# Performance work log

Measured on AMD Instinct MI355X. Metric: run time of the kernel, lower is better.

The kernel has to match this reference:

```python
import jax, jax.numpy as jnp
import numpy as np

B, CQ, CKV, E = 8, 256, 256, 256
H, W = 64, 64
HP, WP = 32, 32


def setup_inputs() -> dict:
    key = jax.random.key(0)
    ks = jax.random.split(key, 6)
    C = jax.random.normal(ks[0], (B, CQ, H, W), dtype=jnp.float32)
    P = jax.random.normal(ks[1], (B, CKV, HP, WP), dtype=jnp.float32)
    # 1x1 conv weights, kaiming-ish scale; stored as [out_ch, in_ch]
    theta_w = jax.random.normal(ks[2], (E, CQ), dtype=jnp.float32) * (1.0 / np.sqrt(CQ))
    phi_w = jax.random.normal(ks[3], (E, CKV), dtype=jnp.float32) * (1.0 / np.sqrt(CKV))
    g_w = jax.random.normal(ks[4], (E, CKV), dtype=jnp.float32) * (1.0 / np.sqrt(CKV))
    out_w = jax.random.normal(ks[5], (CQ, E), dtype=jnp.float32) * (1.0 / np.sqrt(E))
    return {"C": C, "P": P, "theta_w": theta_w, "phi_w": phi_w, "g_w": g_w, "out_w": out_w}


def reference(C, P, theta_w, phi_w, g_w, out_w):
    b, _, h, w = C.shape
    e = theta_w.shape[0]
    # 1x1 convs are channel GEMMs
    theta_C = jnp.einsum('bchw,ec->behw', C, theta_w).reshape(b, e, h * w)   # [B,E,Nq]
    phi_P = jnp.einsum('bchw,ec->behw', P, phi_w).reshape(b, e, -1)          # [B,E,Nkv]
    g_P = jnp.einsum('bchw,ec->behw', P, g_w).reshape(b, e, -1)              # [B,E,Nkv]
    attn = jnp.einsum('ben,bem->bnm', theta_C, phi_P) / (e ** 0.5)           # [B,Nq,Nkv]
    attn = jax.nn.softmax(attn, axis=-1)
    out = jnp.einsum('bem,bnm->ben', g_P, attn).reshape(b, e, h, w)          # [B,E,H,W]
    out = jnp.einsum('behw,ce->bchw', out, out_w)                            # [B,CQ,H,W]
    return jnp.concatenate([C, out], axis=1)
```

## Files before the change

kernel.cpp:

```cpp
#include <hip/hip_runtime.h>


typedef __attribute__((ext_vector_type(8))) short short8;
typedef __attribute__((ext_vector_type(16))) float f32x16;
typedef unsigned short ushort_t;

__device__ __forceinline__ unsigned short f2bf(float f) {
    unsigned int u = __float_as_uint(f);
    u += 0x7FFFu + ((u >> 16) & 1u);
    return (unsigned short)(u >> 16);
}
__device__ __forceinline__ unsigned int pack2bf(float a, float b) {
    return (unsigned int)f2bf(a) | ((unsigned int)f2bf(b) << 16);
}
__device__ __forceinline__ void gload16(const ushort_t* g, ushort_t* l) {
    __builtin_amdgcn_global_load_lds(
        (const __attribute__((address_space(1))) unsigned int*)g,
        (__attribute__((address_space(3))) unsigned int*)l, 16, 0, 0);
}
__device__ __forceinline__ f32x16 zero16() {
    f32x16 z;
#pragma unroll
    for (int i = 0; i < 16; ++i) z[i] = 0.f;
    return z;
}

__global__ __launch_bounds__(256) void ct_cvt(const float* __restrict__ X,
                                              float* __restrict__ outCopy,
                                              ushort_t* __restrict__ xT) {
    const int N = 4096;
    int b = blockIdx.z, c0 = blockIdx.y * 64, n0 = blockIdx.x * 64;
    int t = threadIdx.x;
    __shared__ float Xs[64][68];
    const float* Xb = X + ((size_t)b * 256 + c0) * N + n0;
    int cl = t >> 4, nl = (t & 15) * 4;
#pragma unroll
    for (int ci = 0; ci < 4; ++ci) {
        int c = ci * 16 + cl;
        float4 v = *(const float4*)(Xb + (size_t)c * N + nl);
        *(float4*)&Xs[c][nl] = v;
        *(float4*)(outCopy + (size_t)b * 2097152 + (size_t)(c0 + c) * N + n0 + nl) = v;
    }
    __syncthreads();
    ushort_t* xb = xT + (size_t)b * ((size_t)N * 256);
    int nl2 = t & 63, cgb = t >> 6;
#pragma unroll
    for (int cp = 0; cp < 2; ++cp) {
        int cg = cp * 4 + cgb;
        int cb = c0 + cg * 8;
        int n = n0 + nl2;
        short8 v;
#pragma unroll
        for (int u = 0; u < 8; ++u) v[u] = (short)f2bf(Xs[cg * 8 + u][nl2]);
        size_t i16 = ((size_t)(n >> 5) * 16 + (cb >> 4)) * 64 + ((cb >> 3) & 1) * 32 + (n & 31);
        *(short8*)(xb + i16 * 8) = v;
    }
}

__global__ __launch_bounds__(256) void prep_small(const float* __restrict__ P,
                                                  const float* __restrict__ thw,
                                                  const float* __restrict__ phw,
                                                  const float* __restrict__ ow,
                                                  const float* __restrict__ gw,
                                                  ushort_t* __restrict__ pT,
                                                  ushort_t* __restrict__ thc,
                                                  ushort_t* __restrict__ phc,
                                                  ushort_t* __restrict__ w2c) {
    int blk = blockIdx.x;
    int t = threadIdx.x;
    __shared__ float Xs[64][68];
    if (blk < 512) {
        const int N = 1024;
        int bx = blk & 15, by = (blk >> 4) & 3, b = blk >> 6;
        int n0 = bx * 64, c0 = by * 64;
        const float* Xb = P + ((size_t)b * 256 + c0) * N + n0;
        int cl = t >> 4, nl = (t & 15) * 4;
#pragma unroll
        for (int ci = 0; ci < 4; ++ci) {
            int c = ci * 16 + cl;
            *(float4*)&Xs[c][nl] = *(const float4*)(Xb + (size_t)c * N + nl);
        }
        __syncthreads();
        ushort_t* xb = pT + (size_t)b * ((size_t)N * 256);
        int nl2 = t & 63, cgb = t >> 6;
#pragma unroll
        for (int cp = 0; cp < 2; ++cp) {
            int cg = cp * 4 + cgb;
            int cb = c0 + cg * 8;
            int n = n0 + nl2;
            short8 v;
#pragma unroll
            for (int u = 0; u < 8; ++u) v[u] = (short)f2bf(Xs[cg * 8 + u][nl2]);
            size_t i16 = ((size_t)(n >> 5) * 16 + (cb >> 4)) * 64 + ((cb >> 3) & 1) * 32 + (n & 31);
            *(short8*)(xb + i16 * 8) = v;
        }
    } else if (blk < 1024) {
        int r = blk - 512;
        int which = r >> 8;
        int e = r & 255, c = t;
        const float* src = which ? phw : thw;
        ushort_t* dst = which ? phc : thc;
        int idx = ((((e >> 5) * 16 + (c >> 4)) * 64 + ((c >> 3) & 1) * 32 + (e & 31)) << 3) + (c & 7);
        dst[idx] = f2bf(src[e * 256 + c]);
    } else {
        int c0 = (blk - 1024) * 8;
        float acc[8] = {};
        for (int e = 0; e < 256; ++e) {
            float g = gw[e * 256 + t];
#pragma unroll
            for (int i = 0; i < 8; ++i) acc[i] += ow[(c0 + i) * 256 + e] * g;
        }
#pragma unroll
        for (int i = 0; i < 8; ++i) {
            int c = c0 + i, k = t;
            int idx = ((((c >> 5) * 16 + (k >> 4)) * 64 + ((k >> 3) & 1) * 32 + (c & 31)) << 3) + (k & 7);
            w2c[idx] = f2bf(acc[i]);
        }
    }
}

__global__ __launch_bounds__(256, 2) void proj_mfma(const ushort_t* __restrict__ thc,
                                                    const ushort_t* __restrict__ phc,
                                                    const ushort_t* __restrict__ w2c,
                                                    const ushort_t* __restrict__ cT,
                                                    const ushort_t* __restrict__ pT,
                                                    ushort_t* __restrict__ thetaA,
                                                    ushort_t* __restrict__ phiA,
                                                    ushort_t* __restrict__ gVx) {
    int blk = blockIdx.x;
    int tid = threadIdx.x, lane = tid & 63, wid = tid >> 6;
    int l31 = lane & 31, lh = lane >> 5;
    int role, b, nt;
    const ushort_t *Wc, *xTb;
    ushort_t* outp;
    float scale = 1.f;
    if (blk < 256) {
        role = 0; b = blk & 7; nt = blk >> 3;
        Wc = thc; xTb = cT + (size_t)b * 1048576; outp = thetaA + (size_t)b * 1048576;
        scale = 1.4426950408889634f / 16.0f;
    } else if (blk < 320) {
        int r = blk - 256; role = 1; b = r & 7; nt = r >> 3;
        Wc = phc; xTb = pT + (size_t)b * 262144; outp = phiA + (size_t)b * 262144;
    } else {
        int r = blk - 320; role = 2; b = r & 7; nt = r >> 3;
        Wc = w2c; xTb = pT + (size_t)b * 262144; outp = gVx + (size_t)b * 262144;
    }
    const int n0 = nt * 128 + wid * 32;
    const int ncr = (n0 >> 5) * 16;

    f32x16 o[8];
#pragma unroll
    for (int f = 0; f < 8; ++f) o[f] = zero16();

#pragma unroll
    for (int ks = 0; ks < 16; ++ks) {
        short8 xf = *(const short8*)(xTb + ((size_t)(ncr + ks) * 64 + lane) * 8);
#pragma unroll
        for (int f = 0; f < 8; ++f) {
            short8 wf = *(const short8*)(Wc + ((size_t)(f * 16 + ks) * 64 + lane) * 8);
            o[f] = __builtin_amdgcn_mfma_f32_32x32x16_bf16(wf, xf, o[f], 0, 0, 0);
        }
    }

    if (role < 2) {
#pragma unroll
        for (int f = 0; f < 8; ++f) {
#pragma unroll
            for (int rq = 0; rq < 4; ++rq) {
                uint2 st;
                st.x = pack2bf(o[f][4 * rq + 0] * scale, o[f][4 * rq + 1] * scale);
                st.y = pack2bf(o[f][4 * rq + 2] * scale, o[f][4 * rq + 3] * scale);
                size_t addr = ((size_t)(ncr + f * 2 + (rq >> 1)) * 64 + l31 + 32 * (rq & 1)) * 8 + 4 * lh;
                *(uint2*)(outp + addr) = st;
            }
        }
    } else {
        int kvq = (n0 >> 4) + (l31 >> 4);
        int lhw = 32 * ((l31 >> 3) & 1);
        int kl = l31 & 7;
#pragma unroll
        for (int f = 0; f < 8; ++f) {
#pragma unroll
            for (int r = 0; r < 16; ++r) {
                int crow = (r & 3) + 8 * (r >> 2) + 4 * lh;
                size_t addr = ((size_t)(f * 64 + kvq) * 64 + crow + lhw) * 8 + kl;
                outp[addr] = f2bf(o[f][r]);
            }
        }
    }
}

__global__ __launch_bounds__(512, 2) void attn4(const ushort_t* __restrict__ thetaA,
                                                const ushort_t* __restrict__ phiA,
                                                const ushort_t* __restrict__ gVx,
                                                float* __restrict__ out) {
    const int b = blockIdx.x & 7, qt = blockIdx.x >> 3;
    const int tid = threadIdx.x, lane = tid & 63, wid = tid >> 6;
    const int l31 = lane & 31, lh = lane >> 5;
    const int h = wid >> 2, qg = wid & 3;

    __shared__ __align__(16) ushort_t smem[65536];
    __shared__ float rmS[4][32], rlS[4][32];

    const ushort_t* thA = thetaA + (size_t)b * 1048576;
    const ushort_t* phA = phiA + (size_t)b * 262144;
    const ushort_t* gVb = gVx + (size_t)b * 262144;

    auto stage = [&](int it, int d) {
        if (wid < 2) {
            const ushort_t* src = phA + (size_t)(2 * it) * 8192 + (wid & 1) * 4096 + lane * 8;
            ushort_t* dst = smem + d * 8192 + (wid & 1) * 4096;
#pragma unroll
            for (int i = 0; i < 8; ++i) gload16(src + i * 512, dst + i * 512);
        } else if (wid < 4) {
#pragma unroll
            for (int cg2 = 0; cg2 < 4; ++cg2) {
                int cg = (wid & 1) * 4 + cg2;
#pragma unroll
                for (int j = 0; j < 2; ++j) {
                    const ushort_t* src = gVb + ((size_t)(cg * 64 + 4 * it + j) * 64 + lane) * 8;
                    ushort_t* dst = smem + 16384 + d * 8192 + cg * 1024 + j * 512;
                    gload16(src, dst);
                }
            }
        } else if (wid < 6) {
            const ushort_t* src = phA + (size_t)(2 * it + 1) * 8192 + (wid & 1) * 4096 + lane * 8;
            ushort_t* dst = smem + 32768 + d * 8192 + (wid & 1) * 4096;
#pragma unroll
            for (int i = 0; i < 8; ++i) gload16(src + i * 512, dst + i * 512);
        } else {
#pragma unroll
            for (int cg2 = 0; cg2 < 4; ++cg2) {
                int cg = (wid & 1) * 4 + cg2;
#pragma unroll
                for (int j = 0; j < 2; ++j) {
                    const ushort_t* src = gVb + ((size_t)(cg * 64 + 4 * it + 2 + j) * 64 + lane) * 8;
                    ushort_t* dst = smem + 32768 + 16384 + d * 8192 + cg * 1024 + j * 512;
                    gload16(src, dst);
                }
            }
        }
    };

    stage(0, 0);

    short8 qf[16];
    {
        const int qcr = (qt * 4 + qg) * 16;
#pragma unroll
        for (int ks = 0; ks < 16; ++ks)
            qf[ks] = *(const short8*)(thA + ((size_t)(qcr + ks) * 64 + lane) * 8);
    }

    f32x16 o[8];
#pragma unroll
    for (int f = 0; f < 8; ++f) o[f] = zero16();
    float rm = -1e30f, rl = 0.f;

    for (int it = 0; it < 16; ++it) {
        if (it < 15) {
            stage(it + 1, (it + 1) & 1);
            asm volatile("s_waitcnt vmcnt(8)" ::: "memory");
        } else {
            asm volatile("s_waitcnt vmcnt(0)" ::: "memory");
        }
        __builtin_amdgcn_s_barrier();
        __builtin_amdgcn_sched_barrier(0);

        const int d = it & 1;
        const ushort_t* Kb = smem + h * 32768 + d * 8192;
        const ushort_t* Vb = smem + h * 32768 + 16384 + d * 8192;

        f32x16 s = zero16();
#pragma unroll
        for (int ks = 0; ks < 16; ++ks) {
            short8 kf = *(const short8*)(Kb + (size_t)ks * 512 + lane * 8);
            s = __builtin_amdgcn_mfma_f32_32x32x16_bf16(kf, qf[ks], s, 0, 0, 0);
        }

        float tmax = s[0];
#pragma unroll
        for (int r = 1; r < 16; ++r) tmax = fmaxf(tmax, s[r]);
        tmax = fmaxf(tmax, __shfl_xor(tmax, 32));
        if (!__all(tmax - rm <= 8.f)) {
            float nm = fmaxf(rm, tmax);
            float sc = __builtin_amdgcn_exp2f(rm - nm);
            rl *= sc;
#pragma unroll
            for (int f = 0; f < 8; ++f)
#pragma unroll
                for (int r = 0; r < 16; ++r) o[f][r] *= sc;
            rm = nm;
        }
        float ps = 0.f;
#pragma unroll
        for (int r = 0; r < 16; ++r) {
            s[r] = __builtin_amdgcn_exp2f(s[r] - rm);
            ps += s[r];
        }
        ps += __shfl_xor(ps, 32);
        rl += ps;

        unsigned int a0 = pack2bf(s[0], s[1]),  b0 = pack2bf(s[4], s[5]);
        unsigned int a1 = pack2bf(s[2], s[3]),  b1 = pack2bf(s[6], s[7]);
        unsigned int a2 = pack2bf(s[8], s[9]),  b2 = pack2bf(s[12], s[13]);
        unsigned int a3 = pack2bf(s[10], s[11]), b3 = pack2bf(s[14], s[15]);
        asm volatile("v_permlane32_swap_b32 %0, %1" : "+v"(a0), "+v"(b0));
        asm volatile("v_permlane32_swap_b32 %0, %1" : "+v"(a1), "+v"(b1));
        asm volatile("v_permlane32_swap_b32 %0, %1" : "+v"(a2), "+v"(b2));
        asm volatile("v_permlane32_swap_b32 %0, %1" : "+v"(a3), "+v"(b3));
        union PW { unsigned int u[4]; short8 v; };
        PW p0; p0.u[0] = a0; p0.u[1] = a1; p0.u[2] = b0; p0.u[3] = b1;
        PW p1; p1.u[0] = a2; p1.u[1] = a3; p1.u[2] = b2; p1.u[3] = b3;

#pragma unroll
        for (int ks2 = 0; ks2 < 2; ++ks2) {
            short8 pf = ks2 ? p1.v : p0.v;
#pragma unroll
            for (int f = 0; f < 8; ++f) {
                short8 vf = *(const short8*)(Vb + (size_t)f * 1024 + ks2 * 512 + lane * 8);
                o[f] = __builtin_amdgcn_mfma_f32_32x32x16_bf16(vf, pf, o[f], 0, 0, 0);
            }
        }
        __builtin_amdgcn_sched_barrier(0);
        __builtin_amdgcn_s_barrier();
    }

    if (wid >= 4) {
        float* part = (float*)smem + (size_t)(wid - 4) * 8192;
#pragma unroll
        for (int f = 0; f < 8; ++f)
#pragma unroll
            for (int r = 0; r < 16; ++r) {
                int e = f * 32 + (r & 3) + 8 * (r >> 2) + 4 * lh;
                part[e * 32 + l31] = o[f][r];
            }
        if (lane < 32) { rmS[wid - 4][l31] = rm; rlS[wid - 4][l31] = rl; }
    }
    __syncthreads();
    if (wid < 4) {
        float rm1 = rmS[wid][l31], rl1 = rlS[wid][l31];
        float m = fmaxf(rm, rm1);
        float c0 = __builtin_amdgcn_exp2f(rm - m);
        float c1 = __builtin_amdgcn_exp2f(rm1 - m);
        float inv = 1.f / (rl * c0 + rl1 * c1);
        const float* part = (const float*)smem + (size_t)wid * 8192;
        float* ob = out + (size_t)b * 2097152 + (size_t)256 * 4096 + qt * 128 + qg * 32 + l31;
#pragma unroll
        for (int f = 0; f < 8; ++f)
#pragma unroll
            for (int r = 0; r < 16; ++r) {
                int e = f * 32 + (r & 3) + 8 * (r >> 2) + 4 * lh;
                ob[(size_t)e * 4096] = (o[f][r] * c0 + part[e * 32 + l31] * c1) * inv;
            }
    }
}


extern "C" void kernel_launch(void* const* d_in, const int* in_sizes, int n_in,
                              void* d_out, int out_size, void* d_ws, size_t ws_size,
                              hipStream_t stream) {
    const float* C       = (const float*)d_in[0];
    const float* P       = (const float*)d_in[1];
    const float* theta_w = (const float*)d_in[2];
    const float* phi_w   = (const float*)d_in[3];
    const float* g_w     = (const float*)d_in[4];
    const float* out_w   = (const float*)d_in[5];
    float* out = (float*)d_out;

    ushort_t* ws = (ushort_t*)d_ws;
    ushort_t* thetaA = ws;
    ushort_t* cT     = ws + 8388608;
    ushort_t* phiA   = ws + 16777216;
    ushort_t* pT     = ws + 18874368;
    ushort_t* gVx    = ws + 20971520;
    ushort_t* thWc   = ws + 23068672;
    ushort_t* phWc   = ws + 23134208;
    ushort_t* w2c    = ws + 23199744;

    prep_small<<<1056, 256, 0, stream>>>(P, theta_w, phi_w, out_w, g_w,
                                         pT, thWc, phWc, w2c);
    ct_cvt<<<dim3(64, 4, 8), 256, 0, stream>>>(C, out, cT);
    proj_mfma<<<384, 256, 0, stream>>>(thWc, phWc, w2c, cT, pT, thetaA, phiA, gVx);
    attn4<<<256, 512, 0, stream>>>(thetaA, phiA, gVx, out);
}
```

Before: 127.4 us.

## Software-pipeline QK of next tile with PV of current tile in attention

Restructures the attention kernel so the QK^T MFMAs for the next KV tile are computed one iteration ahead and interleaved with the PV MFMAs for the current tile. K and V staging become separate, with K prefetched two tiles ahead and V one tile ahead. The softmax work can then overlap the matrix units, and s_setprio raises wave priority during the MFMA section. In exchange it keeps an extra score accumulator live, which raises register pressure, and it uses one barrier per iteration with a full vmcnt(0) wait.

```diff
diff --git a/kernel.cpp b/kernel.cpp
--- a/kernel.cpp
+++ b/kernel.cpp
@@ -190,7 +190,7 @@
     }
 }
 
-__global__ __launch_bounds__(512, 2) void attn4(const ushort_t* __restrict__ thetaA,
+__global__ __launch_bounds__(512, 2) void attn6(const ushort_t* __restrict__ thetaA,
                                                 const ushort_t* __restrict__ phiA,
                                                 const ushort_t* __restrict__ gVx,
                                                 float* __restrict__ out) {
@@ -206,43 +206,33 @@
     const ushort_t* phA = phiA + (size_t)b * 262144;
     const ushort_t* gVb = gVx + (size_t)b * 262144;
 
-    auto stage = [&](int it, int d) {
-        if (wid < 2) {
-            const ushort_t* src = phA + (size_t)(2 * it) * 8192 + (wid & 1) * 4096 + lane * 8;
-            ushort_t* dst = smem + d * 8192 + (wid & 1) * 4096;
+    auto stageK = [&](int j) {
+        if ((wid & 2) == 0) {
+            int hh = wid >> 2;
+            const ushort_t* src = phA + (size_t)(2 * j + hh) * 8192 + (wid & 1) * 4096 + lane * 8;
+            ushort_t* dst = smem + hh * 16384 + (j & 1) * 8192 + (wid & 1) * 4096;
 #pragma unroll
             for (int i = 0; i < 8; ++i) gload16(src + i * 512, dst + i * 512);
-        } else if (wid < 4) {
+        }
+    };
+    auto stageV = [&](int j) {
+        if ((wid & 2) == 2) {
+            int hh = wid >> 2;
 #pragma unroll
             for (int cg2 = 0; cg2 < 4; ++cg2) {
                 int cg = (wid & 1) * 4 + cg2;
 #pragma unroll
-                for (int j = 0; j < 2; ++j) {
-                    const ushort_t* src = gVb + ((size_t)(cg * 64 + 4 * it + j) * 64 + lane) * 8;
-                    ushort_t* dst = smem + 16384 + d * 8192 + cg * 1024 + j * 512;
+                for (int jj = 0; jj < 2; ++jj) {
+                    const ushort_t* src =
+                        gVb + ((size_t)(cg * 64 + 4 * j + 2 * hh + jj) * 64 + lane) * 8;
+                    ushort_t* dst = smem + 32768 + hh * 16384 + (j & 1) * 8192 + cg * 1024 + jj * 512;
                     gload16(src, dst);
                 }
             }
-        } else if (wid < 6) {
-            const ushort_t* src = phA + (size_t)(2 * it + 1) * 8192 + (wid & 1) * 4096 + lane * 8;
-            ushort_t* dst = smem + 32768 + d * 8192 + (wid & 1) * 4096;
-#pragma unroll
-            for (int i = 0; i < 8; ++i) gload16(src + i * 512, dst + i * 512);
-        } else {
-#pragma unroll
-            for (int cg2 = 0; cg2 < 4; ++cg2) {
-                int cg = (wid & 1) * 4 + cg2;
-#pragma unroll
-                for (int j = 0; j < 2; ++j) {
-                    const ushort_t* src = gVb + ((size_t)(cg * 64 + 4 * it + 2 + j) * 64 + lane) * 8;
-                    ushort_t* dst = smem + 32768 + 16384 + d * 8192 + cg * 1024 + j * 512;
-                    gload16(src, dst);
-                }
-            }
         }
     };
 
-    stage(0, 0);
+    stageK(0); stageK(1); stageV(0);
 
     short8 qf[16];
     {
@@ -257,26 +247,26 @@
     for (int f = 0; f < 8; ++f) o[f] = zero16();
     float rm = -1e30f, rl = 0.f;
 
-    for (int it = 0; it < 16; ++it) {
-        if (it < 15) {
-            stage(it + 1, (it + 1) & 1);
-            asm volatile("s_waitcnt vmcnt(8)" ::: "memory");
-        } else {
-            asm volatile("s_waitcnt vmcnt(0)" ::: "memory");
-        }
-        __builtin_amdgcn_s_barrier();
-        __builtin_amdgcn_sched_barrier(0);
-
-        const int d = it & 1;
-        const ushort_t* Kb = smem + h * 32768 + d * 8192;
-        const ushort_t* Vb = smem + h * 32768 + 16384 + d * 8192;
-
-        f32x16 s = zero16();
+    asm volatile("s_waitcnt vmcnt(0)" ::: "memory");
+    __builtin_amdgcn_s_barrier();
+    __builtin_amdgcn_sched_barrier(0);
+
+    f32x16 s = zero16();
+    {
+        const ushort_t* Kb = smem + h * 16384;
 #pragma unroll
         for (int ks = 0; ks < 16; ++ks) {
             short8 kf = *(const short8*)(Kb + (size_t)ks * 512 + lane * 8);
             s = __builtin_amdgcn_mfma_f32_32x32x16_bf16(kf, qf[ks], s, 0, 0, 0);
         }
+    }
+
+    for (int it = 0; it < 16; ++it) {
+        asm volatile("s_waitcnt vmcnt(0)" ::: "memory");
+        __builtin_amdgcn_s_barrier();
+        __builtin_amdgcn_sched_barrier(0);
+        if (it < 14) stageK(it + 2);
+        if (it < 15) stageV(it + 1);
 
         float tmax = s[0];
 #pragma unroll
@@ -301,9 +291,9 @@
         ps += __shfl_xor(ps, 32);
         rl += ps;
 
-        unsigned int a0 = pack2bf(s[0], s[1]),  b0 = pack2bf(s[4], s[5]);
-        unsigned int a1 = pack2bf(s[2], s[3]),  b1 = pack2bf(s[6], s[7]);
-        unsigned int a2 = pack2bf(s[8], s[9]),  b2 = pack2bf(s[12], s[13]);
+        unsigned int a0 = pack2bf(s[0], s[1]),   b0 = pack2bf(s[4], s[5]);
+        unsigned int a1 = pack2bf(s[2], s[3]),   b1 = pack2bf(s[6], s[7]);
+        unsigned int a2 = pack2bf(s[8], s[9]),   b2 = pack2bf(s[12], s[13]);
         unsigned int a3 = pack2bf(s[10], s[11]), b3 = pack2bf(s[14], s[15]);
         asm volatile("v_permlane32_swap_b32 %0, %1" : "+v"(a0), "+v"(b0));
         asm volatile("v_permlane32_swap_b32 %0, %1" : "+v"(a1), "+v"(b1));
@@ -313,18 +303,40 @@
         PW p0; p0.u[0] = a0; p0.u[1] = a1; p0.u[2] = b0; p0.u[3] = b1;
         PW p1; p1.u[0] = a2; p1.u[1] = a3; p1.u[2] = b2; p1.u[3] = b3;
 
-#pragma unroll
-        for (int ks2 = 0; ks2 < 2; ++ks2) {
-            short8 pf = ks2 ? p1.v : p0.v;
-#pragma unroll
-            for (int f = 0; f < 8; ++f) {
-                short8 vf = *(const short8*)(Vb + (size_t)f * 1024 + ks2 * 512 + lane * 8);
-                o[f] = __builtin_amdgcn_mfma_f32_32x32x16_bf16(vf, pf, o[f], 0, 0, 0);
-            }
-        }
+        const ushort_t* Vb = smem + 32768 + h * 16384 + (it & 1) * 8192;
+        const ushort_t* Kb = smem + h * 16384 + ((it + 1) & 1) * 8192;
+        __builtin_amdgcn_s_setprio(1);
+        if (it < 15) {
+            f32x16 sn = zero16();
+#pragma unroll
+            for (int ks2 = 0; ks2 < 2; ++ks2) {
+                short8 pf = ks2 ? p1.v : p0.v;
+#pragma unroll
+                for (int f = 0; f < 8; ++f) {
+                    short8 vf = *(const short8*)(Vb + (size_t)f * 1024 + ks2 * 512 + lane * 8);
+                    o[f] = __builtin_amdgcn_mfma_f32_32x32x16_bf16(vf, pf, o[f], 0, 0, 0);
+                    int ks = ks2 * 8 + f;
+                    short8 kf = *(const short8*)(Kb + (size_t)ks * 512 + lane * 8);
+                    sn = __builtin_amdgcn_mfma_f32_32x32x16_bf16(kf, qf[ks], sn, 0, 0, 0);
+                }
+            }
+            s = sn;
+        } else {
+#pragma unroll
+            for (int ks2 = 0; ks2 < 2; ++ks2) {
+                short8 pf = ks2 ? p1.v : p0.v;
+#pragma unroll
+                for (int f = 0; f < 8; ++f) {
+                    short8 vf = *(const short8*)(Vb + (size_t)f * 1024 + ks2 * 512 + lane * 8);
+                    o[f] = __builtin_amdgcn_mfma_f32_32x32x16_bf16(vf, pf, o[f], 0, 0, 0);
+                }
+            }
+        }
+        __builtin_amdgcn_s_setprio(0);
         __builtin_amdgcn_sched_barrier(0);
-        __builtin_amdgcn_s_barrier();
-    }
+    }
+
+    __syncthreads();
 
     if (wid >= 4) {
         float* part = (float*)smem + (size_t)(wid - 4) * 8192;
@@ -382,5 +394,5 @@
                                          pT, thWc, phWc, w2c);
     ct_cvt<<<dim3(64, 4, 8), 256, 0, stream>>>(C, out, cT);
     proj_mfma<<<384, 256, 0, stream>>>(thWc, phWc, w2c, cT, pT, thetaA, phiA, gVx);
-    attn4<<<256, 512, 0, stream>>>(thetaA, phiA, gVx, out);
-}
+    attn6<<<256, 512, 0, stream>>>(thetaA, phiA, gVx, out);
+}
```

Result: faster. 124.7 us (-2.1%).
